# Kernel tuning notes

Measured on AMD Instinct MI355X. Metric: run time of the kernel, lower is better.

Reference implementation:

```python
import jax, jax.numpy as jnp
import numpy as np

BATCH = 262144
N_STEPS = 10  # hard-coded `range(10)` in the original get_cycles


def _euler_to_matrix(e):
    # Standard extrinsic xyz convention: R = Rz(z) @ Ry(y) @ Rx(x)
    x, y, z = e[..., 0], e[..., 1], e[..., 2]
    cx, sx = jnp.cos(x), jnp.sin(x)
    cy, sy = jnp.cos(y), jnp.sin(y)
    cz, sz = jnp.cos(z), jnp.sin(z)
    r0 = jnp.stack([cz * cy, cz * sy * sx - sz * cx, cz * sy * cx + sz * sx], -1)
    r1 = jnp.stack([sz * cy, sz * sy * sx + cz * cx, sz * sy * cx - cz * sx], -1)
    r2 = jnp.stack([-sy, cy * sx, cy * cx], -1)
    return jnp.stack([r0, r1, r2], -2)  # (..., 3, 3)


def _matrix_to_euler(R):
    # Classic rotationMatrixToEulerAngles (inverse of Rz@Ry@Rx), with singular branch
    sy = jnp.sqrt(R[..., 0, 0] ** 2 + R[..., 1, 0] ** 2)
    singular = sy < 1e-6
    x = jnp.where(singular,
                  jnp.arctan2(-R[..., 1, 2], R[..., 1, 1]),
                  jnp.arctan2(R[..., 2, 1], R[..., 2, 2]))
    y = jnp.arctan2(-R[..., 2, 0], sy)
    z = jnp.where(singular, jnp.zeros_like(sy), jnp.arctan2(R[..., 1, 0], R[..., 0, 0]))
    return jnp.stack([x, y, z], -1)


def _get_cycles(x):
    # x: (B, 6*N_STEPS), interleaved [t(3), r(3)] per step (per the original reshape())
    x = jax.lax.stop_gradient(x)  # mirrors .detach().numpy() in the original
    g = x.reshape(x.shape[0], N_STEPS, 6)
    t = g[:, :, :3]   # (B, S, 3) translations
    r = g[:, :, 3:]   # (B, S, 3) euler rotations

    # --- translation part ---
    # The original aliases path_pred[0] onto t[0:3] via .numpy() and mutates it
    # in-place across cycle iterations (j=0 doubles it). The resulting recorded
    # values obey: v_0 = t_0 ; v_i = 2*v_{i-1} + sum_{j=1}^{i-1} t_j
    C = jnp.cumsum(t[:, 1:, :], axis=1)  # C[:, k-1, :] = sum_{j=1..k} t_j
    v = [t[:, 0, :]]
    for i in range(1, N_STEPS):
        tail = C[:, i - 2, :] if i >= 2 else jnp.zeros_like(v[0])
        v.append(2.0 * v[-1] + tail)
    trans = jnp.stack(v, axis=1)  # (B, S, 3)

    # --- rotation part ---
    # numpy `*=` is ELEMENTWISE, so cycle i records
    # matrix_to_euler( R(r_1) * prod_{j<i} R(r_j) )  (Hadamard product)
    R = _euler_to_matrix(r)                    # (B, S, 3, 3)
    CP = jnp.cumprod(R, axis=1)                # CP[:, k] = elemwise prod_{j<=k} R_j
    P = jnp.concatenate([jnp.ones_like(R[:, :1]), CP[:, :-1]], axis=1)  # prod_{j<i}
    M = R[:, 1:2] * P                          # (B, S, 3, 3)
    rot = _matrix_to_euler(M)                  # (B, S, 3)

    return jnp.stack([trans, rot], axis=2)     # (B, S, 2, 3)


def setup_inputs():
    key = jax.random.key(0)
    k1, k2 = jax.random.split(key)
    pred = jax.random.normal(k1, (BATCH, 6 * N_STEPS), dtype=jnp.float32)
    gt = jax.random.normal(k2, (BATCH, 6 * N_STEPS), dtype=jnp.float32)
    return {"pred": pred, "gt": gt}


def reference(pred, gt):
    pred_cycles = _get_cycles(pred)
    gt_cycles = _get_cycles(gt)
    loss = jnp.mean((pred_cycles - gt_cycles) ** 2)
    return loss / BATCH  # original divides the MSE by self.batch_size
```

## Files before the change

kernel.cpp:

```cpp
#include <hip/hip_runtime.h>
#include <math.h>

#define NSTEP 10
#define ROW_U32 31
#define GT_OFF  (32 * ROW_U32)
#define WAVE_U32 (64 * ROW_U32)

typedef __fp16 half2_t __attribute__((ext_vector_type(2)));

__device__ __forceinline__ float fast_atan2f(float y, float x) {
    float ax = fabsf(x), ay = fabsf(y);
    float mx = fmaxf(ax, ay);
    float mn = fminf(ax, ay);
    float a = mn * __builtin_amdgcn_rcpf(mx);
    float s = a * a;
    float r = fmaf(s, fmaf(s, 0.0793312f, -0.2886793f), 0.9953545f) * a;
    if (ay > ax) r = 1.57079632679f - r;
    if (x < 0.0f) r = 3.14159265359f - r;
    return copysignf(r, y);
}

__device__ __forceinline__ void euler2mat5(float x, float y, float z, float R[5]) {
    float sx, cx, sy, cy, sz, cz;
    __sincosf(x, &sx, &cx);
    __sincosf(y, &sy, &cy);
    __sincosf(z, &sz, &cz);
    R[0] = cz * cy;
    R[1] = sz * cy;
    R[2] = -sy;
    R[3] = cy * sx;
    R[4] = cy * cx;
}

__device__ __forceinline__ void emit(float v, float& acc) {
    int pi = __builtin_amdgcn_update_dpp(0, __float_as_int(v), 0xB1, 0xF, 0xF, true);
    float d = v - __int_as_float(pi);
    acc = fmaf(d, d, acc);
}

__device__ __forceinline__ void emit_euler(const float M[5], float& acc) {
    float sy = __builtin_amdgcn_sqrtf(fmaf(M[0], M[0], M[1] * M[1]));
    emit(fast_atan2f(M[3], M[4]), acc);
    emit(fast_atan2f(-M[2], sy), acc);
    emit(fast_atan2f(M[1], M[0]), acc);
}

__device__ __forceinline__ void unpack2(unsigned u, float& lo, float& hi) {
    union { unsigned u; half2_t h; } cv; cv.u = u;
    lo = (float)cv.h.x; hi = (float)cv.h.y;
}

__global__ __launch_bounds__(256) void cycle_loss_main(
    const float* __restrict__ pred, const float* __restrict__ gt,
    float* __restrict__ partial)
{
    __shared__ unsigned lds[4 * WAVE_U32];
    const int tid  = threadIdx.x;
    const int lane = tid & 63;
    const int wid  = tid >> 6;

    {
        const size_t rbase = ((size_t)blockIdx.x * 128 + wid * 32) * 30;
        const float2* pp = reinterpret_cast<const float2*>(pred) + rbase;
        const float2* gp = reinterpret_cast<const float2*>(gt)   + rbase;
        unsigned* lw = lds + wid * WAVE_U32;

        float2 pa[15], ga[15];
        #pragma unroll
        for (int it = 0; it < 15; ++it) {
            pa[it] = pp[lane + 64 * it];
            ga[it] = gp[lane + 64 * it];
        }
        #pragma unroll
        for (int it = 0; it < 15; ++it) {
            unsigned q = (unsigned)lane + 64u * it;
            unsigned idx = q + q / 30u;
            half2_t ha = __builtin_amdgcn_cvt_pkrtz(pa[it].x, pa[it].y);
            half2_t hb = __builtin_amdgcn_cvt_pkrtz(ga[it].x, ga[it].y);
            union { half2_t h; unsigned u; } ca, cb; ca.h = ha; cb.h = hb;
            lw[idx]          = ca.u;
            lw[GT_OFF + idx] = cb.u;
        }
    }

    float acc = 0.0f;
    {
        const unsigned* row = lds + wid * WAVE_U32
                            + ((lane & 1) ? GT_OFF : 0) + (lane >> 1) * ROW_U32;

        float v[3], cac[3] = {0,0,0}, tprev[3];
        float Q[5];

        float e0,e1,e2,e3,e4,e5,e6,e7,e8,e9,e10,e11;
        unpack2(row[0], e0, e1);  unpack2(row[1], e2, e3);
        unpack2(row[2], e4, e5);  unpack2(row[3], e6, e7);
        unpack2(row[4], e8, e9);  unpack2(row[5], e10, e11);

        v[0] = e0; v[1] = e1; v[2] = e2;
        emit(v[0], acc); emit(v[1], acc); emit(v[2], acc);
        #pragma unroll
        for (int k = 0; k < 3; ++k) { v[k] *= 2.0f; emit(v[k], acc); }
        tprev[0] = e6; tprev[1] = e7; tprev[2] = e8;

        {
            float R1[5];
            euler2mat5(e3, e4, e5, Q);
            euler2mat5(e9, e10, e11, R1);
            emit_euler(R1, acc);
            #pragma unroll
            for (int k = 0; k < 5; ++k) Q[k] *= R1[k];
            emit_euler(Q, acc);
            #pragma unroll
            for (int k = 0; k < 5; ++k) Q[k] *= R1[k];
        }

        #pragma unroll
        for (int c = 1; c < 5; ++c) {
            const unsigned* rc = row + 6 * c;
            float f0,f1,f2,f3,f4,f5,f6,f7,f8,f9,f10,f11;
            unpack2(rc[0], f0, f1);  unpack2(rc[1], f2, f3);
            unpack2(rc[2], f4, f5);  unpack2(rc[3], f6, f7);
            unpack2(rc[4], f8, f9);  unpack2(rc[5], f10, f11);

            cac[0] += tprev[0]; cac[1] += tprev[1]; cac[2] += tprev[2];
            #pragma unroll
            for (int k = 0; k < 3; ++k) { v[k] = fmaf(2.0f, v[k], cac[k]); emit(v[k], acc); }
            cac[0] += f0; cac[1] += f1; cac[2] += f2;
            #pragma unroll
            for (int k = 0; k < 3; ++k) { v[k] = fmaf(2.0f, v[k], cac[k]); emit(v[k], acc); }
            tprev[0] = f6; tprev[1] = f7; tprev[2] = f8;

            emit_euler(Q, acc);
            {
                float R[5];
                euler2mat5(f3, f4, f5, R);
                #pragma unroll
                for (int k = 0; k < 5; ++k) Q[k] *= R[k];
            }
            emit_euler(Q, acc);
            if (c < 4) {
                float R[5];
                euler2mat5(f9, f10, f11, R);
                #pragma unroll
                for (int k = 0; k < 5; ++k) Q[k] *= R[k];
            }
        }
    }

    #pragma unroll
    for (int off = 32; off > 0; off >>= 1)
        acc += __shfl_down(acc, off, 64);
    if (lane == 0)
        partial[blockIdx.x * 4 + wid] = acc;
}

__global__ __launch_bounds__(256) void cycle_loss_fin(
    const float* __restrict__ partial, float* __restrict__ out,
    int nparts, float inv)
{
    int t = threadIdx.x;
    float s = 0.0f;
    for (int i = t; i < nparts; i += 256) s += partial[i];
    int lane = t & 63, wid = t >> 6;
    #pragma unroll
    for (int off = 32; off > 0; off >>= 1)
        s += __shfl_down(s, off, 64);
    __shared__ float warp_s[4];
    if (lane == 0) warp_s[wid] = s;
    __syncthreads();
    if (t == 0)
        out[0] = (warp_s[0] + warp_s[1] + warp_s[2] + warp_s[3]) * inv;
}

extern "C" void kernel_launch(void* const* d_in, const int* in_sizes, int n_in,
                              void* d_out, int out_size, void* d_ws, size_t ws_size,
                              hipStream_t stream) {
    const float* pred = (const float*)d_in[0];
    const float* gt   = (const float*)d_in[1];
    int batch = in_sizes[0] / 60;
    float* partial = (float*)d_ws;

    const int threads = 256;
    const int blocks = batch / 128;
    cycle_loss_main<<<blocks, threads, 0, stream>>>(pred, gt, partial);

    double inv = 0.5 / (60.0 * (double)batch * (double)batch);
    cycle_loss_fin<<<1, threads, 0, stream>>>(partial, (float*)d_out, blocks * 4, (float)inv);
}
```

Baseline: 146.2 us.

## Load rows directly from global with float4 prefetch, dropping LDS fp16 staging

Removes the per-wave LDS staging in which coalesced float2 loads were packed to fp16 and then read back per sample. Each thread now reads its own 240-byte row straight from global memory as float4 values, prefetching the next 48-byte chunk while the current one is computed. It also sets a minimum-blocks hint in the launch bounds. This cuts the LDS traffic and the fp16 convert and unpack work, and keeps full fp32 precision. In exchange, global accesses are strided per thread rather than coalesced across the wave, relying on cache lines being reused by later loads.

```diff
diff --git a/kernel.cpp b/kernel.cpp
--- a/kernel.cpp
+++ b/kernel.cpp
@@ -2,11 +2,6 @@
 #include <math.h>
 
 #define NSTEP 10
-#define ROW_U32 31
-#define GT_OFF  (32 * ROW_U32)
-#define WAVE_U32 (64 * ROW_U32)
-
-typedef __fp16 half2_t __attribute__((ext_vector_type(2)));
 
 __device__ __forceinline__ float fast_atan2f(float y, float x) {
     float ax = fabsf(x), ay = fabsf(y);
@@ -45,56 +40,28 @@
     emit(fast_atan2f(M[1], M[0]), acc);
 }
 
-__device__ __forceinline__ void unpack2(unsigned u, float& lo, float& hi) {
-    union { unsigned u; half2_t h; } cv; cv.u = u;
-    lo = (float)cv.h.x; hi = (float)cv.h.y;
-}
-
-__global__ __launch_bounds__(256) void cycle_loss_main(
+__global__ __launch_bounds__(256, 8) void cycle_loss_main(
     const float* __restrict__ pred, const float* __restrict__ gt,
     float* __restrict__ partial)
 {
-    __shared__ unsigned lds[4 * WAVE_U32];
     const int tid  = threadIdx.x;
     const int lane = tid & 63;
     const int wid  = tid >> 6;
 
-    {
-        const size_t rbase = ((size_t)blockIdx.x * 128 + wid * 32) * 30;
-        const float2* pp = reinterpret_cast<const float2*>(pred) + rbase;
-        const float2* gp = reinterpret_cast<const float2*>(gt)   + rbase;
-        unsigned* lw = lds + wid * WAVE_U32;
-
-        float2 pa[15], ga[15];
-        #pragma unroll
-        for (int it = 0; it < 15; ++it) {
-            pa[it] = pp[lane + 64 * it];
-            ga[it] = gp[lane + 64 * it];
-        }
-        #pragma unroll
-        for (int it = 0; it < 15; ++it) {
-            unsigned q = (unsigned)lane + 64u * it;
-            unsigned idx = q + q / 30u;
-            half2_t ha = __builtin_amdgcn_cvt_pkrtz(pa[it].x, pa[it].y);
-            half2_t hb = __builtin_amdgcn_cvt_pkrtz(ga[it].x, ga[it].y);
-            union { half2_t h; unsigned u; } ca, cb; ca.h = ha; cb.h = hb;
-            lw[idx]          = ca.u;
-            lw[GT_OFF + idx] = cb.u;
-        }
-    }
+    const size_t sample = (size_t)blockIdx.x * 128 + (tid >> 1);
+    const float* bp = (tid & 1) ? gt : pred;
+    const float4* rp = reinterpret_cast<const float4*>(bp + sample * 60);
 
     float acc = 0.0f;
+    float v[3], cac[3] = {0.f, 0.f, 0.f}, tprev[3], Q[5];
+
+    float4 A = rp[0], B = rp[1], C = rp[2];
+
     {
-        const unsigned* row = lds + wid * WAVE_U32
-                            + ((lane & 1) ? GT_OFF : 0) + (lane >> 1) * ROW_U32;
-
-        float v[3], cac[3] = {0,0,0}, tprev[3];
-        float Q[5];
-
-        float e0,e1,e2,e3,e4,e5,e6,e7,e8,e9,e10,e11;
-        unpack2(row[0], e0, e1);  unpack2(row[1], e2, e3);
-        unpack2(row[2], e4, e5);  unpack2(row[3], e6, e7);
-        unpack2(row[4], e8, e9);  unpack2(row[5], e10, e11);
+        float4 nA = rp[3], nB = rp[4], nC = rp[5];
+        float e0 = A.x, e1 = A.y, e2 = A.z, e3 = A.w,
+              e4 = B.x, e5 = B.y, e6 = B.z, e7 = B.w,
+              e8 = C.x, e9 = C.y, e10 = C.z, e11 = C.w;
 
         v[0] = e0; v[1] = e1; v[2] = e2;
         emit(v[0], acc); emit(v[1], acc); emit(v[2], acc);
@@ -102,48 +69,50 @@
         for (int k = 0; k < 3; ++k) { v[k] *= 2.0f; emit(v[k], acc); }
         tprev[0] = e6; tprev[1] = e7; tprev[2] = e8;
 
+        float R1[5];
+        euler2mat5(e3, e4, e5, Q);
+        euler2mat5(e9, e10, e11, R1);
+        emit_euler(R1, acc);
+        #pragma unroll
+        for (int k = 0; k < 5; ++k) Q[k] *= R1[k];
+        emit_euler(Q, acc);
+        #pragma unroll
+        for (int k = 0; k < 5; ++k) Q[k] *= R1[k];
+
+        A = nA; B = nB; C = nC;
+    }
+
+    #pragma unroll
+    for (int c = 1; c < 5; ++c) {
+        float4 nA, nB, nC;
+        if (c < 4) { nA = rp[3*c + 3]; nB = rp[3*c + 4]; nC = rp[3*c + 5]; }
+        float f0 = A.x, f1 = A.y, f2 = A.z, f3 = A.w,
+              f4 = B.x, f5 = B.y, f6 = B.z, f7 = B.w,
+              f8 = C.x, f9 = C.y, f10 = C.z, f11 = C.w;
+        (void)f4; (void)f5;
+
+        cac[0] += tprev[0]; cac[1] += tprev[1]; cac[2] += tprev[2];
+        #pragma unroll
+        for (int k = 0; k < 3; ++k) { v[k] = fmaf(2.0f, v[k], cac[k]); emit(v[k], acc); }
+        cac[0] += f0; cac[1] += f1; cac[2] += f2;
+        #pragma unroll
+        for (int k = 0; k < 3; ++k) { v[k] = fmaf(2.0f, v[k], cac[k]); emit(v[k], acc); }
+        tprev[0] = f6; tprev[1] = f7; tprev[2] = f8;
+
+        emit_euler(Q, acc);
         {
-            float R1[5];
-            euler2mat5(e3, e4, e5, Q);
-            euler2mat5(e9, e10, e11, R1);
-            emit_euler(R1, acc);
+            float R[5];
+            euler2mat5(f3, f4, f5, R);
             #pragma unroll
-            for (int k = 0; k < 5; ++k) Q[k] *= R1[k];
-            emit_euler(Q, acc);
+            for (int k = 0; k < 5; ++k) Q[k] *= R[k];
+        }
+        emit_euler(Q, acc);
+        if (c < 4) {
+            float R[5];
+            euler2mat5(f9, f10, f11, R);
             #pragma unroll
-            for (int k = 0; k < 5; ++k) Q[k] *= R1[k];
-        }
-
-        #pragma unroll
-        for (int c = 1; c < 5; ++c) {
-            const unsigned* rc = row + 6 * c;
-            float f0,f1,f2,f3,f4,f5,f6,f7,f8,f9,f10,f11;
-            unpack2(rc[0], f0, f1);  unpack2(rc[1], f2, f3);
-            unpack2(rc[2], f4, f5);  unpack2(rc[3], f6, f7);
-            unpack2(rc[4], f8, f9);  unpack2(rc[5], f10, f11);
-
-            cac[0] += tprev[0]; cac[1] += tprev[1]; cac[2] += tprev[2];
-            #pragma unroll
-            for (int k = 0; k < 3; ++k) { v[k] = fmaf(2.0f, v[k], cac[k]); emit(v[k], acc); }
-            cac[0] += f0; cac[1] += f1; cac[2] += f2;
-            #pragma unroll
-            for (int k = 0; k < 3; ++k) { v[k] = fmaf(2.0f, v[k], cac[k]); emit(v[k], acc); }
-            tprev[0] = f6; tprev[1] = f7; tprev[2] = f8;
-
-            emit_euler(Q, acc);
-            {
-                float R[5];
-                euler2mat5(f3, f4, f5, R);
-                #pragma unroll
-                for (int k = 0; k < 5; ++k) Q[k] *= R[k];
-            }
-            emit_euler(Q, acc);
-            if (c < 4) {
-                float R[5];
-                euler2mat5(f9, f10, f11, R);
-                #pragma unroll
-                for (int k = 0; k < 5; ++k) Q[k] *= R[k];
-            }
+            for (int k = 0; k < 5; ++k) Q[k] *= R[k];
+            A = nA; B = nB; C = nC;
         }
     }
 
```

Measured after the change: 153.7 us. 5.1% more time.
